# Optimization experiments

Hardware: AMD Instinct MI355X
Metric: run time of the kernel (lower is better)

The kernel has to match this reference:

```python
import jax, jax.numpy as jnp
import numpy as np

EPS = 1e-06

def quant4(x):
    # per-row (last dim) symmetric 4-bit quant with straight-through estimator
    max_abs = jax.lax.stop_gradient(jnp.max(jnp.abs(x), axis=-1, keepdims=True))
    max_abs = jnp.maximum(max_abs, EPS)
    q = jnp.clip(jnp.round(x / max_abs * 7.0), -8.0, 7.0)
    deq = q * max_abs / 7.0
    # forward value = deq, gradient = identity w.r.t. x
    return x + jax.lax.stop_gradient(deq - x)

def ternary_weight(w):
    thresh = 0.05 * jnp.mean(jnp.abs(w))
    sign = jnp.where(jnp.abs(w) < thresh, 0.0, jnp.sign(w))
    alpha = jnp.mean(jnp.abs(w), axis=1, keepdims=True)  # per output row scale
    tern = sign * alpha
    # forward value = tern, gradient = identity w.r.t. w
    return w + jax.lax.stop_gradient(tern - w)

def setup_inputs() -> dict:
    key = jax.random.key(0)
    kx, kw = jax.random.split(key)
    B, S, IN_F, OUT_F = 8, 4096, 1024, 1024
    x = jax.random.normal(kx, (B, S, IN_F), dtype=jnp.float32)
    weight = jax.random.normal(kw, (OUT_F, IN_F), dtype=jnp.float32) / np.sqrt(IN_F)
    bias = jnp.zeros((OUT_F,), dtype=jnp.float32)
    return {"x": x, "weight": weight, "bias": bias}

def reference(x, weight, bias):
    xq = quant4(x)                       # [B, S, in_f]
    wq = ternary_weight(weight)          # [out_f, in_f]
    out = jnp.einsum('bsi,oi->bso', xq, wq) + bias
    return out
```

## Files before the change

### kernel.cpp

```cpp
#include <hip/hip_runtime.h>
#include <hip/hip_bf16.h>


typedef __attribute__((ext_vector_type(4))) int int32x4;

#define IN_F 1024
#define OUT_F 1024

__device__ inline float waveMax(float v) {
#pragma unroll
    for (int off = 32; off > 0; off >>= 1) v = fmaxf(v, __shfl_xor(v, off, 64));
    return v;
}
__device__ inline float waveSum(float v) {
#pragma unroll
    for (int off = 32; off > 0; off >>= 1) v += __shfl_xor(v, off, 64);
    return v;
}

__device__ inline unsigned int pack4(int a, int b, int c, int d) {
    return (unsigned)(a & 255) | ((unsigned)(b & 255) << 8) |
           ((unsigned)(c & 255) << 16) | ((unsigned)(d & 255) << 24);
}

__global__ __launch_bounds__(256) void wsum_kernel(const float* __restrict__ w,
                                                   float* __restrict__ alpha) {
    __shared__ float red[4];
    const int row = blockIdx.x;
    const int tid = threadIdx.x;
    float4 v = reinterpret_cast<const float4*>(w + (size_t)row * IN_F)[tid];
    float s = fabsf(v.x) + fabsf(v.y) + fabsf(v.z) + fabsf(v.w);
    s = waveSum(s);
    if ((tid & 63) == 0) red[tid >> 6] = s;
    __syncthreads();
    if (tid == 0)
        alpha[row] = (red[0] + red[1] + red[2] + red[3]) * (1.0f / (float)IN_F);
}

__global__ __launch_bounds__(256) void wquant_kernel(const float* __restrict__ w,
                                                     const float* __restrict__ alpha,
                                                     signed char* __restrict__ wq) {
    __shared__ float red[4];
    const int tid = threadIdx.x;
    float4 a = reinterpret_cast<const float4*>(alpha)[tid];
    float s = a.x + a.y + a.z + a.w;
    s = waveSum(s);
    if ((tid & 63) == 0) red[tid >> 6] = s;
    __syncthreads();
    const float thresh =
        0.05f * ((red[0] + red[1] + red[2] + red[3]) * (1.0f / (float)OUT_F));

    const int row = blockIdx.x;
    float4 v = reinterpret_cast<const float4*>(w + (size_t)row * IN_F)[tid];
    int s0 = (fabsf(v.x) < thresh) ? 0 : (v.x > 0.0f ? 1 : -1);
    int s1 = (fabsf(v.y) < thresh) ? 0 : (v.y > 0.0f ? 1 : -1);
    int s2 = (fabsf(v.z) < thresh) ? 0 : (v.z > 0.0f ? 1 : -1);
    int s3 = (fabsf(v.w) < thresh) ? 0 : (v.w > 0.0f ? 1 : -1);
    reinterpret_cast<unsigned int*>(wq)[(size_t)row * (IN_F / 4) + tid] =
        pack4(s0, s1, s2, s3);
}

__global__ __launch_bounds__(256) void quantx_kernel(const float* __restrict__ x,
                                                     signed char* __restrict__ xq,
                                                     float* __restrict__ sx) {
    __shared__ float red[4];
    const int row = blockIdx.x;
    const int tid = threadIdx.x;
    float4 v = reinterpret_cast<const float4*>(x + (size_t)row * IN_F)[tid];
    float m = fmaxf(fmaxf(fabsf(v.x), fabsf(v.y)), fmaxf(fabsf(v.z), fabsf(v.w)));
    m = waveMax(m);
    if ((tid & 63) == 0) red[tid >> 6] = m;
    __syncthreads();
    m = fmaxf(fmaxf(red[0], red[1]), fmaxf(red[2], red[3]));
    m = fmaxf(m, 1e-6f);
    float t0 = fminf(fmaxf(rintf((v.x / m) * 7.0f), -8.0f), 7.0f);
    float t1 = fminf(fmaxf(rintf((v.y / m) * 7.0f), -8.0f), 7.0f);
    float t2 = fminf(fmaxf(rintf((v.z / m) * 7.0f), -8.0f), 7.0f);
    float t3 = fminf(fmaxf(rintf((v.w / m) * 7.0f), -8.0f), 7.0f);
    reinterpret_cast<unsigned int*>(xq)[(size_t)row * (IN_F / 4) + tid] =
        pack4((int)t0, (int)t1, (int)t2, (int)t3);
    if (tid == 0) sx[row] = m / 7.0f;
}

__global__ __launch_bounds__(256) void gemm_kernel(
    const signed char* __restrict__ xq, const signed char* __restrict__ wq,
    const float* __restrict__ sx, const float* __restrict__ alpha,
    const float* __restrict__ bias, float* __restrict__ out) {
    const int nwg = gridDim.x;
    int bid = blockIdx.x;
    if ((nwg & 7) == 0) bid = (bid & 7) * (nwg >> 3) + (bid >> 3);
    const int bn = bid & 7;
    const int bm = bid >> 3;

    const int lane = threadIdx.x & 63;
    const int wid = threadIdx.x >> 6;
    const int m_w = bm * 128 + (wid >> 1) * 64;
    const int n_w = bn * 128 + (wid & 1) * 64;
    const int fr = lane & 15;
    const int koff = (lane >> 4) * 16;

    const signed char* ap = xq + (size_t)(m_w + fr) * IN_F + koff;
    const signed char* bp = wq + (size_t)(n_w + fr) * IN_F + koff;

    int32x4 acc[4][4];
#pragma unroll
    for (int i = 0; i < 4; ++i)
#pragma unroll
        for (int j = 0; j < 4; ++j) acc[i][j] = (int32x4){0, 0, 0, 0};

    for (int k0 = 0; k0 < IN_F; k0 += 64) {
        int32x4 afr[4], bfr[4];
#pragma unroll
        for (int i = 0; i < 4; ++i)
            afr[i] = *reinterpret_cast<const int32x4*>(ap + (size_t)i * 16 * IN_F + k0);
#pragma unroll
        for (int j = 0; j < 4; ++j)
            bfr[j] = *reinterpret_cast<const int32x4*>(bp + (size_t)j * 16 * IN_F + k0);
#pragma unroll
        for (int i = 0; i < 4; ++i)
#pragma unroll
            for (int j = 0; j < 4; ++j)
                acc[i][j] = __builtin_amdgcn_mfma_i32_16x16x64_i8(afr[i], bfr[j],
                                                                  acc[i][j], 0, 0, 0);
    }

    const int crow = (lane >> 4) * 4;
    const int ccol = lane & 15;
#pragma unroll
    for (int j = 0; j < 4; ++j) {
        const int n = n_w + j * 16 + ccol;
        const float al = alpha[n];
        const float bs = bias[n];
#pragma unroll
        for (int i = 0; i < 4; ++i) {
            const int mbase = m_w + i * 16 + crow;
#pragma unroll
            for (int rr = 0; rr < 4; ++rr) {
                const int m = mbase + rr;
                out[(size_t)m * OUT_F + n] =
                    (float)acc[i][j][rr] * (sx[m] * al) + bs;
            }
        }
    }
}

extern "C" void kernel_launch(void* const* d_in, const int* in_sizes, int n_in,
                              void* d_out, int out_size, void* d_ws, size_t ws_size,
                              hipStream_t stream) {
    const float* x = (const float*)d_in[0];
    const float* w = (const float*)d_in[1];
    const float* bias = (const float*)d_in[2];
    float* out = (float*)d_out;
    const int M = in_sizes[0] / IN_F;

    char* ws = (char*)d_ws;
    signed char* xq = (signed char*)ws;
    signed char* wq = xq + (size_t)M * IN_F;
    float* sx = (float*)(wq + (size_t)OUT_F * IN_F);
    float* alpha = sx + M;

    wsum_kernel<<<OUT_F, 256, 0, stream>>>(w, alpha);
    wquant_kernel<<<OUT_F, 256, 0, stream>>>(w, alpha, wq);
    quantx_kernel<<<M, 256, 0, stream>>>(x, xq, sx);
    gemm_kernel<<<(M / 128) * (OUT_F / 128), 256, 0, stream>>>(xq, wq, sx, alpha,
                                                               bias, out);
}
```

Measured before the change: 348.8 us.

## Double-buffer GEMM fragment loads, wave-per-row x quant, nontemporal IO

The GEMM main loop is fully unrolled and register double-buffered, so the next k-step's A/B fragments load while MFMAs run on the current ones. The x quantization kernel now gives each 64-lane wave its own row, which removes the LDS reduction and block barrier, and it reads x with nontemporal loads. The GEMM epilogue writes the output with nontemporal stores. Together these aim to hide global load latency and cut cache pollution from streaming data, at the cost of more VGPRs from the doubled fragment buffers.

New measurement: 346.5 us. About the same (-0.7%).

```diff
diff --git a/kernel.cpp b/kernel.cpp
--- a/kernel.cpp
+++ b/kernel.cpp
@@ -3,6 +3,7 @@
 
 
 typedef __attribute__((ext_vector_type(4))) int int32x4;
+typedef __attribute__((ext_vector_type(4))) float f32x4;
 
 #define IN_F 1024
 #define OUT_F 1024
@@ -28,7 +29,7 @@
     __shared__ float red[4];
     const int row = blockIdx.x;
     const int tid = threadIdx.x;
-    float4 v = reinterpret_cast<const float4*>(w + (size_t)row * IN_F)[tid];
+    f32x4 v = reinterpret_cast<const f32x4*>(w + (size_t)row * IN_F)[tid];
     float s = fabsf(v.x) + fabsf(v.y) + fabsf(v.z) + fabsf(v.w);
     s = waveSum(s);
     if ((tid & 63) == 0) red[tid >> 6] = s;
@@ -42,7 +43,7 @@
                                                      signed char* __restrict__ wq) {
     __shared__ float red[4];
     const int tid = threadIdx.x;
-    float4 a = reinterpret_cast<const float4*>(alpha)[tid];
+    f32x4 a = reinterpret_cast<const f32x4*>(alpha)[tid];
     float s = a.x + a.y + a.z + a.w;
     s = waveSum(s);
     if ((tid & 63) == 0) red[tid >> 6] = s;
@@ -51,7 +52,7 @@
         0.05f * ((red[0] + red[1] + red[2] + red[3]) * (1.0f / (float)OUT_F));
 
     const int row = blockIdx.x;
-    float4 v = reinterpret_cast<const float4*>(w + (size_t)row * IN_F)[tid];
+    f32x4 v = reinterpret_cast<const f32x4*>(w + (size_t)row * IN_F)[tid];
     int s0 = (fabsf(v.x) < thresh) ? 0 : (v.x > 0.0f ? 1 : -1);
     int s1 = (fabsf(v.y) < thresh) ? 0 : (v.y > 0.0f ? 1 : -1);
     int s2 = (fabsf(v.z) < thresh) ? 0 : (v.z > 0.0f ? 1 : -1);
@@ -63,23 +64,31 @@
 __global__ __launch_bounds__(256) void quantx_kernel(const float* __restrict__ x,
                                                      signed char* __restrict__ xq,
                                                      float* __restrict__ sx) {
-    __shared__ float red[4];
-    const int row = blockIdx.x;
-    const int tid = threadIdx.x;
-    float4 v = reinterpret_cast<const float4*>(x + (size_t)row * IN_F)[tid];
-    float m = fmaxf(fmaxf(fabsf(v.x), fabsf(v.y)), fmaxf(fabsf(v.z), fabsf(v.w)));
+    const int row = blockIdx.x * 4 + (threadIdx.x >> 6);
+    const int lane = threadIdx.x & 63;
+    const f32x4* xr = reinterpret_cast<const f32x4*>(x + (size_t)row * IN_F);
+
+    f32x4 v[4];
+    float m = 0.0f;
+#pragma unroll
+    for (int j = 0; j < 4; ++j) {
+        v[j] = __builtin_nontemporal_load(&xr[lane + 64 * j]);
+        m = fmaxf(m, fmaxf(fmaxf(fabsf(v[j].x), fabsf(v[j].y)),
+                           fmaxf(fabsf(v[j].z), fabsf(v[j].w))));
+    }
     m = waveMax(m);
-    if ((tid & 63) == 0) red[tid >> 6] = m;
-    __syncthreads();
-    m = fmaxf(fmaxf(red[0], red[1]), fmaxf(red[2], red[3]));
     m = fmaxf(m, 1e-6f);
-    float t0 = fminf(fmaxf(rintf((v.x / m) * 7.0f), -8.0f), 7.0f);
-    float t1 = fminf(fmaxf(rintf((v.y / m) * 7.0f), -8.0f), 7.0f);
-    float t2 = fminf(fmaxf(rintf((v.z / m) * 7.0f), -8.0f), 7.0f);
-    float t3 = fminf(fmaxf(rintf((v.w / m) * 7.0f), -8.0f), 7.0f);
-    reinterpret_cast<unsigned int*>(xq)[(size_t)row * (IN_F / 4) + tid] =
-        pack4((int)t0, (int)t1, (int)t2, (int)t3);
-    if (tid == 0) sx[row] = m / 7.0f;
+
+    unsigned int* xqr = reinterpret_cast<unsigned int*>(xq + (size_t)row * IN_F);
+#pragma unroll
+    for (int j = 0; j < 4; ++j) {
+        float t0 = fminf(fmaxf(rintf((v[j].x / m) * 7.0f), -8.0f), 7.0f);
+        float t1 = fminf(fmaxf(rintf((v[j].y / m) * 7.0f), -8.0f), 7.0f);
+        float t2 = fminf(fmaxf(rintf((v[j].z / m) * 7.0f), -8.0f), 7.0f);
+        float t3 = fminf(fmaxf(rintf((v[j].w / m) * 7.0f), -8.0f), 7.0f);
+        xqr[lane + 64 * j] = pack4((int)t0, (int)t1, (int)t2, (int)t3);
+    }
+    if (lane == 0) sx[row] = m * (1.0f / 7.0f);
 }
 
 __global__ __launch_bounds__(256) void gemm_kernel(
@@ -108,20 +117,34 @@
 #pragma unroll
         for (int j = 0; j < 4; ++j) acc[i][j] = (int32x4){0, 0, 0, 0};
 
-    for (int k0 = 0; k0 < IN_F; k0 += 64) {
-        int32x4 afr[4], bfr[4];
+    int32x4 afr[2][4], bfr[2][4];
 #pragma unroll
-        for (int i = 0; i < 4; ++i)
-            afr[i] = *reinterpret_cast<const int32x4*>(ap + (size_t)i * 16 * IN_F + k0);
+    for (int i = 0; i < 4; ++i)
+        afr[0][i] = *reinterpret_cast<const int32x4*>(ap + (size_t)i * 16 * IN_F);
 #pragma unroll
-        for (int j = 0; j < 4; ++j)
-            bfr[j] = *reinterpret_cast<const int32x4*>(bp + (size_t)j * 16 * IN_F + k0);
+    for (int j = 0; j < 4; ++j)
+        bfr[0][j] = *reinterpret_cast<const int32x4*>(bp + (size_t)j * 16 * IN_F);
+
+#pragma unroll
+    for (int t = 0; t < 16; ++t) {
+        const int cur = t & 1, nxt = cur ^ 1;
+        if (t < 15) {
+            const int k1 = (t + 1) * 64;
+#pragma unroll
+            for (int i = 0; i < 4; ++i)
+                afr[nxt][i] = *reinterpret_cast<const int32x4*>(
+                    ap + (size_t)i * 16 * IN_F + k1);
+#pragma unroll
+            for (int j = 0; j < 4; ++j)
+                bfr[nxt][j] = *reinterpret_cast<const int32x4*>(
+                    bp + (size_t)j * 16 * IN_F + k1);
+        }
 #pragma unroll
         for (int i = 0; i < 4; ++i)
 #pragma unroll
             for (int j = 0; j < 4; ++j)
-                acc[i][j] = __builtin_amdgcn_mfma_i32_16x16x64_i8(afr[i], bfr[j],
-                                                                  acc[i][j], 0, 0, 0);
+                acc[i][j] = __builtin_amdgcn_mfma_i32_16x16x64_i8(
+                    afr[cur][i], bfr[cur][j], acc[i][j], 0, 0, 0);
     }
 
     const int crow = (lane >> 4) * 4;
@@ -137,8 +160,9 @@
 #pragma unroll
             for (int rr = 0; rr < 4; ++rr) {
                 const int m = mbase + rr;
-                out[(size_t)m * OUT_F + n] =
-                    (float)acc[i][j][rr] * (sx[m] * al) + bs;
+                __builtin_nontemporal_store(
+                    (float)acc[i][j][rr] * (sx[m] * al) + bs,
+                    &out[(size_t)m * OUT_F + n]);
             }
         }
     }
@@ -161,7 +185,7 @@
 
     wsum_kernel<<<OUT_F, 256, 0, stream>>>(w, alpha);
     wquant_kernel<<<OUT_F, 256, 0, stream>>>(w, alpha, wq);
-    quantx_kernel<<<M, 256, 0, stream>>>(x, xq, sx);
+    quantx_kernel<<<M / 4, 256, 0, stream>>>(x, xq, sx);
     gemm_kernel<<<(M / 128) * (OUT_F / 128), 256, 0, stream>>>(xq, wq, sx, alpha,
                                                                bias, out);
 }
```
